# Optimization experiments

Measured on AMD Instinct MI355X. Metric: run time of the kernel, lower is better.

Reference implementation:

```python
import jax, jax.numpy as jnp
import numpy as np

N_NODES = 100000
N_EDGES = 1600000
DIMS = [256, 128, 64, 32, 16]  # halving pyramid from number_of_x=256 down to number_of_classes=16
N_LAYERS = len(DIMS) - 1


def setup_inputs() -> dict:
    key = jax.random.key(0)
    ks = jax.random.split(key, 3 + N_LAYERS)
    inp = {
        "x": jax.random.normal(ks[0], (N_NODES, DIMS[0]), jnp.float32),
        "src": jax.random.randint(ks[1], (N_EDGES,), 0, N_NODES),
        "dst": jax.random.randint(ks[2], (N_EDGES,), 0, N_NODES),
    }
    for i in range(N_LAYERS):
        inp[f"W{i}"] = jax.random.normal(ks[3 + i], (DIMS[i], DIMS[i + 1]), jnp.float32) / np.sqrt(DIMS[i])
        inp[f"b{i}"] = jnp.zeros((DIMS[i + 1],), jnp.float32)   # GraphConv bias
        inp[f"sb{i}"] = jnp.zeros((1,), jnp.float32)            # module's extra scalar bias
    return inp


def _gcn_layer(h, src, dst, W, b, norm_src, norm_dst):
    # DGL GraphConv, norm='both', in_feats >= out_feats -> transform first, then aggregate
    h = h * norm_src[:, None]                                    # D_out^{-1/2} * X
    h = h @ W                                                    # GEMM
    agg = jax.ops.segment_sum(h[src], dst, num_segments=N_NODES) # SpMM aggregation
    return agg * norm_dst[:, None] + b                           # D_in^{-1/2}, + bias


def reference(x, src, dst, W0, b0, sb0, W1, b1, sb1, W2, b2, sb2, W3, b3, sb3):
    ones = jnp.ones((N_EDGES,), jnp.float32)
    out_deg = jax.ops.segment_sum(ones, src, num_segments=N_NODES)
    in_deg = jax.ops.segment_sum(ones, dst, num_segments=N_NODES)
    norm_src = jnp.maximum(out_deg, 1.0) ** -0.5
    norm_dst = jnp.maximum(in_deg, 1.0) ** -0.5
    h = x
    for W, b, sb in ((W0, b0, sb0), (W1, b1, sb1), (W2, b2, sb2), (W3, b3, sb3)):
        h = jax.nn.relu(_gcn_layer(h, src, dst, W, b, norm_src, norm_dst) + sb)
    return jax.nn.softmax(h, axis=1)
```

## Files before the change

### kernel.cpp

```cpp
#include <hip/hip_runtime.h>
#include <hip/hip_bf16.h>

#define N_NODES 100000
#define N_EDGES 1600000

typedef unsigned short u16;
typedef unsigned int u32;

static __device__ __forceinline__ u16 f2bf(float f) {
    union { float f; u32 u; } v; v.f = f;
    u32 u = v.u;
    u += 0x7FFFu + ((u >> 16) & 1u);
    return (u16)(u >> 16);
}
static __device__ __forceinline__ float bflo(u32 w) {
    union { u32 u; float f; } v; v.u = w << 16; return v.f;
}
static __device__ __forceinline__ float bfhi(u32 w) {
    union { u32 u; float f; } v; v.u = w & 0xFFFF0000u; return v.f;
}

__global__ __launch_bounds__(256) void degree_kernel(
    const int* __restrict__ src, const int* __restrict__ dst,
    u32* __restrict__ shist, u32* __restrict__ dhist, u32* __restrict__ pos) {
    int e = blockIdx.x * 256 + threadIdx.x;
    if (e < N_EDGES) {
        atomicAdd(&shist[src[e]], 1u);
        pos[e] = atomicAdd(&dhist[dst[e]], 1u);
    }
}

__global__ __launch_bounds__(256) void norm_kernel(
    const u32* __restrict__ dhist, const u32* __restrict__ shist,
    float* __restrict__ norm_src, float* __restrict__ norm_dst) {
    int n = blockIdx.x * 256 + threadIdx.x;
    if (n >= N_NODES) return;
    u32 id = dhist[n], od = shist[n];
    norm_dst[n] = rsqrtf((float)(id < 1u ? 1u : id));
    norm_src[n] = rsqrtf((float)(od < 1u ? 1u : od));
}

#define SCAN_B 512
#define SCAN_NBLK ((N_NODES + SCAN_B - 1) / SCAN_B)

__global__ __launch_bounds__(SCAN_B) void scan1_kernel(
    const u32* __restrict__ indeg, u32* __restrict__ row_ptr, u32* __restrict__ bsum) {
    __shared__ u32 s[SCAN_B];
    int t = threadIdx.x;
    int gid = blockIdx.x * SCAN_B + t;
    u32 v = (gid < N_NODES) ? indeg[gid] : 0u;
    s[t] = v;
    __syncthreads();
    for (int off = 1; off < SCAN_B; off <<= 1) {
        u32 x = (t >= off) ? s[t - off] : 0u;
        __syncthreads();
        s[t] += x;
        __syncthreads();
    }
    if (gid < N_NODES) row_ptr[gid + 1] = s[t];
    if (t == SCAN_B - 1) bsum[blockIdx.x] = s[t];
}

__global__ __launch_bounds__(256) void scan2_kernel(u32* __restrict__ bsum, u32* __restrict__ boff) {
    __shared__ u32 s[256];
    int t = threadIdx.x;
    s[t] = (t < SCAN_NBLK) ? bsum[t] : 0u;
    __syncthreads();
    for (int off = 1; off < 256; off <<= 1) {
        u32 x = (t >= off) ? s[t - off] : 0u;
        __syncthreads();
        s[t] += x;
        __syncthreads();
    }
    if (t < SCAN_NBLK) boff[t] = (t == 0) ? 0u : s[t - 1];
}

__global__ __launch_bounds__(256) void scan3_kernel(u32* __restrict__ row_ptr, const u32* __restrict__ boff) {
    int gid = blockIdx.x * 256 + threadIdx.x;
    if (gid < N_NODES) {
        row_ptr[gid + 1] += boff[gid / SCAN_B];
        if (gid == 0) row_ptr[0] = 0u;
    }
}

__global__ __launch_bounds__(256) void fill_kernel(
    const int* __restrict__ src, const int* __restrict__ dst,
    const u32* __restrict__ row_ptr, const u32* __restrict__ pos,
    u32* __restrict__ col) {
    int e = blockIdx.x * 256 + threadIdx.x;
    if (e < N_EDGES) {
        int d = dst[e];
        col[row_ptr[d] + pos[e]] = (u32)src[e];
    }
}

template <int DIN, int DOUT>
__global__ __launch_bounds__(256) void gemm_kernel(
    const float* __restrict__ h, const float* __restrict__ W,
    const float* __restrict__ norm_src, u16* __restrict__ T) {
    constexpr int TM = 64;
    constexpr int KT = 32;
    constexpr int JBLKS = DOUT / 4;
    constexpr int NPT = (TM * DOUT) / (256 * 4);

    __shared__ float hs[KT][TM + 4];
    __shared__ float ws[KT][DOUT];

    const int t = threadIdx.x;
    const int m0 = blockIdx.x * TM;
    const int jblk = t % JBLKS;
    const int nblk = t / JBLKS;
    const int n0 = nblk * NPT;

    float acc[NPT][4];
    for (int i = 0; i < NPT; ++i)
        for (int j = 0; j < 4; ++j) acc[i][j] = 0.f;

    for (int k0 = 0; k0 < DIN; k0 += KT) {
        for (int it = 0; it < 2; ++it) {
            int f = t + it * 256;
            int row = f / (KT / 4);
            int c4  = f % (KT / 4);
            float4 v = make_float4(0.f, 0.f, 0.f, 0.f);
            int gr = m0 + row;
            if (gr < N_NODES)
                v = *reinterpret_cast<const float4*>(&h[gr * DIN + k0 + c4 * 4]);
            hs[c4 * 4 + 0][row] = v.x;
            hs[c4 * 4 + 1][row] = v.y;
            hs[c4 * 4 + 2][row] = v.z;
            hs[c4 * 4 + 3][row] = v.w;
        }
        constexpr int WQ = KT * DOUT / 4;
        constexpr int WITERS = (WQ + 255) / 256;
        for (int it = 0; it < WITERS; ++it) {
            int f = t + it * 256;
            if (f < WQ) {
                int row = f / JBLKS;
                int c4  = f % JBLKS;
                *reinterpret_cast<float4*>(&ws[row][c4 * 4]) =
                    *reinterpret_cast<const float4*>(&W[(k0 + row) * DOUT + c4 * 4]);
            }
        }
        __syncthreads();

#pragma unroll 4
        for (int k = 0; k < KT; ++k) {
            float4 wv = *reinterpret_cast<const float4*>(&ws[k][jblk * 4]);
            float a[NPT];
            if constexpr (NPT % 4 == 0) {
#pragma unroll
                for (int i = 0; i < NPT; i += 4)
                    *reinterpret_cast<float4*>(&a[i]) =
                        *reinterpret_cast<const float4*>(&hs[k][n0 + i]);
            } else if constexpr (NPT == 2) {
                *reinterpret_cast<float2*>(&a[0]) =
                    *reinterpret_cast<const float2*>(&hs[k][n0]);
            } else {
                a[0] = hs[k][n0];
            }
#pragma unroll
            for (int i = 0; i < NPT; ++i) {
                acc[i][0] = fmaf(a[i], wv.x, acc[i][0]);
                acc[i][1] = fmaf(a[i], wv.y, acc[i][1]);
                acc[i][2] = fmaf(a[i], wv.z, acc[i][2]);
                acc[i][3] = fmaf(a[i], wv.w, acc[i][3]);
            }
        }
        __syncthreads();
    }

#pragma unroll
    for (int i = 0; i < NPT; ++i) {
        int n = m0 + n0 + i;
        if (n < N_NODES) {
            float s = norm_src[n];
            ushort4 o;
            o.x = f2bf(acc[i][0] * s);
            o.y = f2bf(acc[i][1] * s);
            o.z = f2bf(acc[i][2] * s);
            o.w = f2bf(acc[i][3] * s);
            *reinterpret_cast<ushort4*>(&T[n * DOUT + jblk * 4]) = o;
        }
    }
}

template <int D>
__global__ __launch_bounds__(256) void pull_kernel(
    const u16* __restrict__ T, const u32* __restrict__ row_ptr,
    const u32* __restrict__ col, const float* __restrict__ norm_dst,
    const float* __restrict__ b, const float* __restrict__ sb,
    float* __restrict__ h) {
    constexpr int TPN = D / 8;
    int tid = blockIdx.x * 256 + threadIdx.x;
    int n = tid / TPN;
    int c = (tid % TPN) * 8;
    if (n >= N_NODES) return;

    u32 beg = row_ptr[n], end = row_ptr[n + 1];
    float a[8];
#pragma unroll
    for (int j = 0; j < 8; ++j) a[j] = 0.f;

    u32 e = beg;
    for (; e + 1 < end; e += 2) {
        u32 s0 = col[e], s1 = col[e + 1];
        uint4 q0 = *reinterpret_cast<const uint4*>(&T[s0 * D + c]);
        uint4 q1 = *reinterpret_cast<const uint4*>(&T[s1 * D + c]);
        a[0] += bflo(q0.x) + bflo(q1.x);
        a[1] += bfhi(q0.x) + bfhi(q1.x);
        a[2] += bflo(q0.y) + bflo(q1.y);
        a[3] += bfhi(q0.y) + bfhi(q1.y);
        a[4] += bflo(q0.z) + bflo(q1.z);
        a[5] += bfhi(q0.z) + bfhi(q1.z);
        a[6] += bflo(q0.w) + bflo(q1.w);
        a[7] += bfhi(q0.w) + bfhi(q1.w);
    }
    if (e < end) {
        uint4 q0 = *reinterpret_cast<const uint4*>(&T[col[e] * D + c]);
        a[0] += bflo(q0.x); a[1] += bfhi(q0.x);
        a[2] += bflo(q0.y); a[3] += bfhi(q0.y);
        a[4] += bflo(q0.z); a[5] += bfhi(q0.z);
        a[6] += bflo(q0.w); a[7] += bfhi(q0.w);
    }

    float nd = norm_dst[n];
    float sv = sb[0];
    float4 b0 = *reinterpret_cast<const float4*>(&b[c]);
    float4 b1 = *reinterpret_cast<const float4*>(&b[c + 4]);
    float4 o0, o1;
    o0.x = fmaxf(a[0] * nd + b0.x + sv, 0.f);
    o0.y = fmaxf(a[1] * nd + b0.y + sv, 0.f);
    o0.z = fmaxf(a[2] * nd + b0.z + sv, 0.f);
    o0.w = fmaxf(a[3] * nd + b0.w + sv, 0.f);
    o1.x = fmaxf(a[4] * nd + b1.x + sv, 0.f);
    o1.y = fmaxf(a[5] * nd + b1.y + sv, 0.f);
    o1.z = fmaxf(a[6] * nd + b1.z + sv, 0.f);
    o1.w = fmaxf(a[7] * nd + b1.w + sv, 0.f);
    *reinterpret_cast<float4*>(&h[n * D + c])     = o0;
    *reinterpret_cast<float4*>(&h[n * D + c + 4]) = o1;
}

__global__ __launch_bounds__(256) void pull16_sm_kernel(
    const u16* __restrict__ T, const u32* __restrict__ row_ptr,
    const u32* __restrict__ col, const float* __restrict__ norm_dst,
    const float* __restrict__ b, const float* __restrict__ sb,
    float* __restrict__ out) {
    int tid = blockIdx.x * 256 + threadIdx.x;
    int n = tid >> 1;
    int c = (tid & 1) * 8;
    if (n >= N_NODES) return;

    u32 beg = row_ptr[n], end = row_ptr[n + 1];
    float a[8];
#pragma unroll
    for (int j = 0; j < 8; ++j) a[j] = 0.f;

    u32 e = beg;
    for (; e + 1 < end; e += 2) {
        u32 s0 = col[e], s1 = col[e + 1];
        uint4 q0 = *reinterpret_cast<const uint4*>(&T[s0 * 16 + c]);
        uint4 q1 = *reinterpret_cast<const uint4*>(&T[s1 * 16 + c]);
        a[0] += bflo(q0.x) + bflo(q1.x);
        a[1] += bfhi(q0.x) + bfhi(q1.x);
        a[2] += bflo(q0.y) + bflo(q1.y);
        a[3] += bfhi(q0.y) + bfhi(q1.y);
        a[4] += bflo(q0.z) + bflo(q1.z);
        a[5] += bfhi(q0.z) + bfhi(q1.z);
        a[6] += bflo(q0.w) + bflo(q1.w);
        a[7] += bfhi(q0.w) + bfhi(q1.w);
    }
    if (e < end) {
        uint4 q0 = *reinterpret_cast<const uint4*>(&T[col[e] * 16 + c]);
        a[0] += bflo(q0.x); a[1] += bfhi(q0.x);
        a[2] += bflo(q0.y); a[3] += bfhi(q0.y);
        a[4] += bflo(q0.z); a[5] += bfhi(q0.z);
        a[6] += bflo(q0.w); a[7] += bfhi(q0.w);
    }

    float nd = norm_dst[n];
    float sv = sb[0];
    float4 b0 = *reinterpret_cast<const float4*>(&b[c]);
    float4 b1 = *reinterpret_cast<const float4*>(&b[c + 4]);
    float o[8];
    o[0] = fmaxf(a[0] * nd + b0.x + sv, 0.f);
    o[1] = fmaxf(a[1] * nd + b0.y + sv, 0.f);
    o[2] = fmaxf(a[2] * nd + b0.z + sv, 0.f);
    o[3] = fmaxf(a[3] * nd + b0.w + sv, 0.f);
    o[4] = fmaxf(a[4] * nd + b1.x + sv, 0.f);
    o[5] = fmaxf(a[5] * nd + b1.y + sv, 0.f);
    o[6] = fmaxf(a[6] * nd + b1.z + sv, 0.f);
    o[7] = fmaxf(a[7] * nd + b1.w + sv, 0.f);

    float m = o[0];
#pragma unroll
    for (int j = 1; j < 8; ++j) m = fmaxf(m, o[j]);
    m = fmaxf(m, __shfl_xor(m, 1));
    float s = 0.f;
#pragma unroll
    for (int j = 0; j < 8; ++j) { o[j] = __expf(o[j] - m); s += o[j]; }
    s += __shfl_xor(s, 1);
    float inv = 1.f / s;
    float4 w0 = make_float4(o[0] * inv, o[1] * inv, o[2] * inv, o[3] * inv);
    float4 w1 = make_float4(o[4] * inv, o[5] * inv, o[6] * inv, o[7] * inv);
    *reinterpret_cast<float4*>(&out[n * 16 + c])     = w0;
    *reinterpret_cast<float4*>(&out[n * 16 + c + 4]) = w1;
}

extern "C" void kernel_launch(void* const* d_in, const int* in_sizes, int n_in,
                              void* d_out, int out_size, void* d_ws, size_t ws_size,
                              hipStream_t stream) {
    const float* x   = (const float*)d_in[0];
    const int*   src = (const int*)d_in[1];
    const int*   dst = (const int*)d_in[2];
    const float* W0 = (const float*)d_in[3];
    const float* b0 = (const float*)d_in[4];
    const float* sb0 = (const float*)d_in[5];
    const float* W1 = (const float*)d_in[6];
    const float* b1 = (const float*)d_in[7];
    const float* sb1 = (const float*)d_in[8];
    const float* W2 = (const float*)d_in[9];
    const float* b2 = (const float*)d_in[10];
    const float* sb2 = (const float*)d_in[11];
    const float* W3 = (const float*)d_in[12];
    const float* b3 = (const float*)d_in[13];
    const float* sb3 = (const float*)d_in[14];

    char* ws = (char*)d_ws;
    float* h        = (float*)ws;
    u16*   T        = (u16*)(ws + 51200000);
    u32*   dhist    = (u32*)(ws + 51200000);
    u32*   shist    = (u32*)(ws + 51600000);
    u32*   pos      = (u32*)(ws + 52000000);
    u32*   col      = (u32*)(ws + 76800000);
    u32*   row_ptr  = (u32*)(ws + 83200000);
    float* norm_src = (float*)(ws + 83600016);
    float* norm_dst = (float*)(ws + 84000016);
    u32*   bsum     = (u32*)(ws + 84400016);
    u32*   boff     = (u32*)(ws + 84404016);

    const int EB = (N_EDGES + 255) / 256;
    const int NB = (N_NODES + 255) / 256;
    const int MT = (N_NODES + 63) / 64;

    hipMemsetAsync(dhist, 0, 2 * N_NODES * 4, stream);
    degree_kernel<<<EB, 256, 0, stream>>>(src, dst, shist, dhist, pos);
    norm_kernel<<<NB, 256, 0, stream>>>(dhist, shist, norm_src, norm_dst);
    scan1_kernel<<<SCAN_NBLK, SCAN_B, 0, stream>>>(dhist, row_ptr, bsum);
    scan2_kernel<<<1, 256, 0, stream>>>(bsum, boff);
    scan3_kernel<<<NB, 256, 0, stream>>>(row_ptr, boff);
    fill_kernel<<<EB, 256, 0, stream>>>(src, dst, row_ptr, pos, col);

    gemm_kernel<256, 128><<<MT, 256, 0, stream>>>(x, W0, norm_src, T);
    pull_kernel<128><<<(N_NODES * 16 + 255) / 256, 256, 0, stream>>>(T, row_ptr, col, norm_dst, b0, sb0, h);

    gemm_kernel<128, 64><<<MT, 256, 0, stream>>>(h, W1, norm_src, T);
    pull_kernel<64><<<(N_NODES * 8 + 255) / 256, 256, 0, stream>>>(T, row_ptr, col, norm_dst, b1, sb1, h);

    gemm_kernel<64, 32><<<MT, 256, 0, stream>>>(h, W2, norm_src, T);
    pull_kernel<32><<<(N_NODES * 4 + 255) / 256, 256, 0, stream>>>(T, row_ptr, col, norm_dst, b2, sb2, h);

    gemm_kernel<32, 16><<<MT, 256, 0, stream>>>(h, W3, norm_src, T);
    pull16_sm_kernel<<<(N_NODES * 2 + 255) / 256, 256, 0, stream>>>(T, row_ptr, col, norm_dst, b3, sb3, (float*)d_out);
}
```

Measured before the change: 617.3 us.

## Replace global-atomic degree counting and CSR fill with shared-memory sliced histograms

Degree counting and CSR construction now use per-block LDS histograms over node ranges and edge slices instead of global atomics per edge. A prep kernel reduces the slices into degrees, norms and per-slice exclusive offsets, and the fill kernel places column indices using LDS atomics plus those offsets. This removes the global atomic contention and the memset. In exchange, every block reads its whole edge slice for each of the 16 node ranges, which multiplies src/dst reads, and the slice buffers add extra memory traffic.

```diff
diff --git a/kernel.cpp b/kernel.cpp
--- a/kernel.cpp
+++ b/kernel.cpp
@@ -3,6 +3,11 @@
 
 #define N_NODES 100000
 #define N_EDGES 1600000
+#define NRANGE 16
+#define NSLICE 32
+#define RSZ (N_NODES / NRANGE)
+#define ESL (N_EDGES / NSLICE)
+#define EQ (ESL / 4)
 
 typedef unsigned short u16;
 typedef unsigned int u32;
@@ -20,24 +25,57 @@
     union { u32 u; float f; } v; v.u = w & 0xFFFF0000u; return v.f;
 }
 
-__global__ __launch_bounds__(256) void degree_kernel(
+__global__ __launch_bounds__(256) void hist_kernel(
     const int* __restrict__ src, const int* __restrict__ dst,
-    u32* __restrict__ shist, u32* __restrict__ dhist, u32* __restrict__ pos) {
-    int e = blockIdx.x * 256 + threadIdx.x;
-    if (e < N_EDGES) {
-        atomicAdd(&shist[src[e]], 1u);
-        pos[e] = atomicAdd(&dhist[dst[e]], 1u);
-    }
-}
-
-__global__ __launch_bounds__(256) void norm_kernel(
-    const u32* __restrict__ dhist, const u32* __restrict__ shist,
-    float* __restrict__ norm_src, float* __restrict__ norm_dst) {
+    u32* __restrict__ dslice, u32* __restrict__ sslice) {
+    __shared__ u32 db[RSZ];
+    __shared__ u32 sb[RSZ];
+    const int t = threadIdx.x;
+    const int r = blockIdx.x & (NRANGE - 1);
+    const int s = blockIdx.x >> 4;
+    const u32 r0 = (u32)r * RSZ;
+    for (int i = t; i < RSZ; i += 256) { db[i] = 0u; sb[i] = 0u; }
+    __syncthreads();
+    const int e0 = s * ESL;
+    for (int k = t; k < EQ; k += 256) {
+        int idx = e0 + k * 4;
+        uint4 d4 = *reinterpret_cast<const uint4*>(&dst[idx]);
+        uint4 s4 = *reinterpret_cast<const uint4*>(&src[idx]);
+        u32 li;
+        li = d4.x - r0; if (li < RSZ) atomicAdd(&db[li], 1u);
+        li = d4.y - r0; if (li < RSZ) atomicAdd(&db[li], 1u);
+        li = d4.z - r0; if (li < RSZ) atomicAdd(&db[li], 1u);
+        li = d4.w - r0; if (li < RSZ) atomicAdd(&db[li], 1u);
+        li = s4.x - r0; if (li < RSZ) atomicAdd(&sb[li], 1u);
+        li = s4.y - r0; if (li < RSZ) atomicAdd(&sb[li], 1u);
+        li = s4.z - r0; if (li < RSZ) atomicAdd(&sb[li], 1u);
+        li = s4.w - r0; if (li < RSZ) atomicAdd(&sb[li], 1u);
+    }
+    __syncthreads();
+    u32* dbase = dslice + (size_t)(r * NSLICE + s) * RSZ;
+    u32* sbase = sslice + (size_t)(r * NSLICE + s) * RSZ;
+    for (int i = t; i < RSZ; i += 256) { dbase[i] = db[i]; sbase[i] = sb[i]; }
+}
+
+__global__ __launch_bounds__(256) void prep_kernel(
+    u32* __restrict__ dslice, const u32* __restrict__ sslice,
+    u32* __restrict__ indeg, float* __restrict__ norm_src, float* __restrict__ norm_dst) {
     int n = blockIdx.x * 256 + threadIdx.x;
     if (n >= N_NODES) return;
-    u32 id = dhist[n], od = shist[n];
-    norm_dst[n] = rsqrtf((float)(id < 1u ? 1u : id));
-    norm_src[n] = rsqrtf((float)(od < 1u ? 1u : od));
+    int r = n / RSZ;
+    int i = n - r * RSZ;
+    size_t base = (size_t)(r * NSLICE) * RSZ + i;
+    u32 accd = 0u, accs = 0u;
+#pragma unroll
+    for (int s = 0; s < NSLICE; ++s) {
+        u32 c = dslice[base + (size_t)s * RSZ];
+        dslice[base + (size_t)s * RSZ] = accd;
+        accd += c;
+        accs += sslice[base + (size_t)s * RSZ];
+    }
+    indeg[n] = accd;
+    norm_dst[n] = rsqrtf((float)(accd < 1u ? 1u : accd));
+    norm_src[n] = rsqrtf((float)(accs < 1u ? 1u : accs));
 }
 
 #define SCAN_B 512
@@ -83,14 +121,28 @@
     }
 }
 
-__global__ __launch_bounds__(256) void fill_kernel(
+__global__ __launch_bounds__(256) void fill2_kernel(
     const int* __restrict__ src, const int* __restrict__ dst,
-    const u32* __restrict__ row_ptr, const u32* __restrict__ pos,
+    const u32* __restrict__ row_ptr, const u32* __restrict__ dslice,
     u32* __restrict__ col) {
-    int e = blockIdx.x * 256 + threadIdx.x;
-    if (e < N_EDGES) {
-        int d = dst[e];
-        col[row_ptr[d] + pos[e]] = (u32)src[e];
+    __shared__ u32 cur[RSZ];
+    const int t = threadIdx.x;
+    const int r = blockIdx.x & (NRANGE - 1);
+    const int s = blockIdx.x >> 4;
+    const u32 r0 = (u32)r * RSZ;
+    const u32* dbase = dslice + (size_t)(r * NSLICE + s) * RSZ;
+    for (int i = t; i < RSZ; i += 256) cur[i] = 0u;
+    __syncthreads();
+    const int e0 = s * ESL;
+    for (int k = t; k < EQ; k += 256) {
+        int idx = e0 + k * 4;
+        uint4 d4 = *reinterpret_cast<const uint4*>(&dst[idx]);
+        uint4 s4 = *reinterpret_cast<const uint4*>(&src[idx]);
+        u32 li, rk;
+        li = d4.x - r0; if (li < RSZ) { rk = atomicAdd(&cur[li], 1u); col[row_ptr[d4.x] + dbase[li] + rk] = s4.x; }
+        li = d4.y - r0; if (li < RSZ) { rk = atomicAdd(&cur[li], 1u); col[row_ptr[d4.y] + dbase[li] + rk] = s4.y; }
+        li = d4.z - r0; if (li < RSZ) { rk = atomicAdd(&cur[li], 1u); col[row_ptr[d4.z] + dbase[li] + rk] = s4.z; }
+        li = d4.w - r0; if (li < RSZ) { rk = atomicAdd(&cur[li], 1u); col[row_ptr[d4.w] + dbase[li] + rk] = s4.w; }
     }
 }
 
@@ -328,27 +380,25 @@
     char* ws = (char*)d_ws;
     float* h        = (float*)ws;
     u16*   T        = (u16*)(ws + 51200000);
-    u32*   dhist    = (u32*)(ws + 51200000);
-    u32*   shist    = (u32*)(ws + 51600000);
-    u32*   pos      = (u32*)(ws + 52000000);
+    u32*   dslice   = (u32*)(ws + 51200000);
+    u32*   sslice   = (u32*)(ws + 64000000);
     u32*   col      = (u32*)(ws + 76800000);
     u32*   row_ptr  = (u32*)(ws + 83200000);
     float* norm_src = (float*)(ws + 83600016);
     float* norm_dst = (float*)(ws + 84000016);
     u32*   bsum     = (u32*)(ws + 84400016);
     u32*   boff     = (u32*)(ws + 84404016);
-
-    const int EB = (N_EDGES + 255) / 256;
+    u32*   indeg    = (u32*)(ws + 84408016);
+
     const int NB = (N_NODES + 255) / 256;
     const int MT = (N_NODES + 63) / 64;
 
-    hipMemsetAsync(dhist, 0, 2 * N_NODES * 4, stream);
-    degree_kernel<<<EB, 256, 0, stream>>>(src, dst, shist, dhist, pos);
-    norm_kernel<<<NB, 256, 0, stream>>>(dhist, shist, norm_src, norm_dst);
-    scan1_kernel<<<SCAN_NBLK, SCAN_B, 0, stream>>>(dhist, row_ptr, bsum);
+    hist_kernel<<<NRANGE * NSLICE, 256, 0, stream>>>(src, dst, dslice, sslice);
+    prep_kernel<<<NB, 256, 0, stream>>>(dslice, sslice, indeg, norm_src, norm_dst);
+    scan1_kernel<<<SCAN_NBLK, SCAN_B, 0, stream>>>(indeg, row_ptr, bsum);
     scan2_kernel<<<1, 256, 0, stream>>>(bsum, boff);
     scan3_kernel<<<NB, 256, 0, stream>>>(row_ptr, boff);
-    fill_kernel<<<EB, 256, 0, stream>>>(src, dst, row_ptr, pos, col);
+    fill2_kernel<<<NRANGE * NSLICE, 256, 0, stream>>>(src, dst, row_ptr, dslice, col);
 
     gemm_kernel<256, 128><<<MT, 256, 0, stream>>>(x, W0, norm_src, T);
     pull_kernel<128><<<(N_NODES * 16 + 255) / 256, 256, 0, stream>>>(T, row_ptr, col, norm_dst, b0, sb0, h);
```

Result: faster. 572.8 us (-7.2%).
